# Performance work log

Measured on AMD Instinct MI355X. Metric: run time of the kernel, lower is better.

## Reference

```python
import jax, jax.numpy as jnp
import numpy as np

N_NODES = 100000
N_REL = 8
N_EDGES = 80000
IN_F, HID, OUT = 128, 32, 2
N_GRAPHS = 64


def setup_inputs() -> dict:
    key = jax.random.key(0)
    ks = jax.random.split(key, 12)
    x = jax.random.normal(ks[0], (N_NODES, IN_F), dtype=jnp.float32)
    src = jax.random.randint(ks[1], (N_REL, N_EDGES), 0, N_NODES, dtype=jnp.int32)
    dst = jax.random.randint(ks[2], (N_REL, N_EDGES), 0, N_NODES, dtype=jnp.int32)
    graph_ids = jax.random.randint(ks[3], (N_NODES,), 0, N_GRAPHS, dtype=jnp.int32)
    W1 = jax.random.normal(ks[4], (N_REL, IN_F, HID), dtype=jnp.float32) / np.sqrt(IN_F)
    b1 = jnp.zeros((N_REL, HID), dtype=jnp.float32)
    W2 = jax.random.normal(ks[5], (N_REL, HID, HID), dtype=jnp.float32) / np.sqrt(HID)
    b2 = jnp.zeros((N_REL, HID), dtype=jnp.float32)
    Wc = jax.random.normal(ks[6], (HID, OUT), dtype=jnp.float32) / np.sqrt(HID)
    bc = jnp.zeros((OUT,), dtype=jnp.float32)
    return {"x": x, "src": src, "dst": dst, "graph_ids": graph_ids,
            "num_graphs": N_GRAPHS, "W1": W1, "b1": b1, "W2": W2, "b2": b2,
            "Wc": Wc, "bc": bc}


def _hetero_conv(h, src, dst, W, b, n_nodes):
    """HeteroGraphConv(sum) of per-relation GraphConv(norm='both')."""
    n_rel = W.shape[0]
    out = jnp.zeros((n_nodes, W.shape[2]), dtype=h.dtype)
    ones_e = jnp.ones((src.shape[1],), dtype=h.dtype)
    for r in range(n_rel):  # small fixed relation set
        s, d = src[r], dst[r]
        # symmetric normalization with degree clamped to >= 1 (DGL behavior)
        deg_out = jnp.maximum(jax.ops.segment_sum(ones_e, s, num_segments=n_nodes), 1.0)
        deg_in = jnp.maximum(jax.ops.segment_sum(ones_e, d, num_segments=n_nodes), 1.0)
        hn = h * jax.lax.rsqrt(deg_out)[:, None]      # [N, F_in]
        hw = hn @ W[r]                                # project first (F_in >= F_out)
        agg = jax.ops.segment_sum(hw[s], d, num_segments=n_nodes)  # scatter-sum to dst
        out = out + agg * jax.lax.rsqrt(deg_in)[:, None] + b[r]
    return out


def reference(x, src, dst, graph_ids, num_graphs, W1, b1, W2, b2, Wc, bc):
    n = x.shape[0]
    h = jax.nn.relu(_hetero_conv(x, src, dst, W1, b1, n))
    h = _hetero_conv(h, src, dst, W2, b2, n)
    # per-graph mean pooling over nodes
    sums = jax.ops.segment_sum(h, graph_ids, num_segments=num_graphs)
    cnts = jnp.maximum(jax.ops.segment_sum(jnp.ones((n,), h.dtype), graph_ids,
                                           num_segments=num_graphs), 1.0)
    pooled = sums / cnts[:, None]
    return pooled @ Wc + bc
```

## Files before the change

kernel.cpp:

```cpp
#include <hip/hip_runtime.h>


#define N_NODES 100000
#define N_REL   8
#define N_EDGES 80000
#define IN_F    128
#define HID     32
#define N_GRAPHS 64
#define NCAT    (N_REL * HID)
#define N_KEYS  (N_NODES * N_REL)
#define TOT_E   (N_REL * N_EDGES)
#define DEG_BLOCKS  (TOT_E / 256)
#define GEMM_BLOCKS ((N_NODES / 16 + 3) / 4)
#define GID_BLOCKS  ((N_NODES + 1023) / 1024)

constexpr int TILE = 256;
constexpr int KC   = 32;

typedef __attribute__((ext_vector_type(8))) short bf16x8;
typedef __attribute__((ext_vector_type(4))) float f32x4;

__device__ __forceinline__ ushort f2bf(float v) {
  unsigned u = __builtin_bit_cast(unsigned, v);
  u = (u + 0x7fffu + ((u >> 16) & 1u)) >> 16;
  return (ushort)u;
}
__device__ __forceinline__ float bf2f(ushort h) {
  unsigned u = ((unsigned)h) << 16;
  return __builtin_bit_cast(float, u);
}

__global__ __launch_bounds__(256) void rsqrt_kernel(float* __restrict__ p, int count) {
  int i = blockIdx.x * 256 + threadIdx.x;
  if (i < count) {
    int d = ((const int*)p)[i];
    p[i] = rsqrtf((float)(d < 1 ? 1 : d));
  }
}

__global__ __launch_bounds__(256) void prep_w_kernel(const float* __restrict__ W1, const float* __restrict__ W2,
                                                     const float* __restrict__ Wc,
                                                     ushort* __restrict__ Wt1, ushort* __restrict__ Vt) {
  int i = blockIdx.x * 256 + threadIdx.x;
  if (i < NCAT * IN_F) {
    int n = i >> 7, k = i & 127;
    int r = n >> 5, j = n & 31;
    Wt1[i] = f2bf(W1[r * (IN_F * HID) + k * HID + j]);
  } else {
    int q = i - NCAT * IN_F;
    if (q < 16 * HID) {
      int n = q >> 5, k = q & 31;
      int r = n >> 1, c = n & 1;
      float s = 0.f;
#pragma unroll
      for (int j = 0; j < HID; j++) s += W2[r * (HID * HID) + k * HID + j] * Wc[j * 2 + c];
      Vt[q] = f2bf(s);
    }
  }
}

__global__ __launch_bounds__(256, 4) void fused_deg_gemm1(const int* __restrict__ src, const int* __restrict__ dst,
                                                          int* __restrict__ dego, int* __restrict__ cnt,
                                                          int* __restrict__ epos,
                                                          const float* __restrict__ A, const ushort* __restrict__ Bt,
                                                          ushort* __restrict__ Y, int M,
                                                          const int* __restrict__ gid, float* __restrict__ gcnt) {
  __shared__ ushort smem[17408];
  int bid = blockIdx.x;
  int role, rid;
  if (bid < 2 * GEMM_BLOCKS) { role = bid & 1; rid = bid >> 1; }
  else if (bid < GEMM_BLOCKS + DEG_BLOCKS) { role = 1; rid = GEMM_BLOCKS + (bid - 2 * GEMM_BLOCKS); }
  else { role = 2; rid = bid - (GEMM_BLOCKS + DEG_BLOCKS); }

  if (role == 1) {
    int i = rid * 256 + (int)threadIdx.x;
    int s = src[i], d = dst[i];
    int r = i / N_EDGES;
    atomicAdd(&dego[r * N_NODES + s], 1);
    epos[i] = atomicAdd(&cnt[d * N_REL + r], 1);
    return;
  }
  if (role == 2) {
    int* gh = (int*)smem;
    int t = threadIdx.x;
    if (t < N_GRAPHS) gh[t] = 0;
    __syncthreads();
    int base = rid * 1024;
#pragma unroll
    for (int k = 0; k < 4; k++) {
      int n = base + k * 256 + t;
      if (n < N_NODES) atomicAdd(&gh[gid[n]], 1);
    }
    __syncthreads();
    if (t < N_GRAPHS) atomicAdd(&gcnt[t], (float)gh[t]);
    return;
  }

  int wave = __builtin_amdgcn_readfirstlane(threadIdx.x >> 6);
  int lane = threadIdx.x & 63;
  int t = threadIdx.x;
  int m0 = (rid * 4 + wave) * 16;
  int me = (m0 <= M - 16) ? m0 : (M - 16);
  int row = lane & 15, quad = lane >> 4;

  bf16x8 af[4];
#pragma unroll
  for (int kq = 0; kq < 4; kq++) {
    const float* ap = &A[(size_t)(me + row) * IN_F + kq * 32 + quad * 8];
    float4 a0 = *(const float4*)ap;
    float4 a1 = *(const float4*)(ap + 4);
    bf16x8 a;
    a[0] = (short)f2bf(a0.x); a[1] = (short)f2bf(a0.y); a[2] = (short)f2bf(a0.z); a[3] = (short)f2bf(a0.w);
    a[4] = (short)f2bf(a1.x); a[5] = (short)f2bf(a1.y); a[6] = (short)f2bf(a1.z); a[7] = (short)f2bf(a1.w);
    af[kq] = a;
  }

  f32x4 acc[16];
#pragma unroll
  for (int nt = 0; nt < 16; nt++) acc[nt] = (f32x4){0.f, 0.f, 0.f, 0.f};

  for (int p = 0; p < 2; p++) {
    __syncthreads();
    const ushort* bsrc = Bt + (size_t)p * (128 * IN_F);
#pragma unroll
    for (int i = 0; i < 8; i++) {
      int c = t + i * 256;
      int rr2 = c >> 4, cc = c & 15;
      uint4 v = *(const uint4*)&bsrc[rr2 * IN_F + cc * 8];
      *(uint4*)&smem[rr2 * 136 + cc * 8] = v;
    }
    __syncthreads();
#pragma unroll
    for (int kq = 0; kq < 4; kq++) {
#pragma unroll
      for (int nt2 = 0; nt2 < 8; nt2++) {
        bf16x8 b = *(const bf16x8*)&smem[(nt2 * 16 + row) * 136 + kq * 32 + quad * 8];
        acc[p * 8 + nt2] = __builtin_amdgcn_mfma_f32_16x16x32_bf16(af[kq], b, acc[p * 8 + nt2], 0, 0, 0);
      }
    }
  }
  __syncthreads();

  ushort* myt = &smem[wave * 4160];
#pragma unroll
  for (int nt = 0; nt < 16; nt++) {
#pragma unroll
    for (int i = 0; i < 4; i++)
      myt[(quad * 4 + i) * 260 + nt * 16 + row] = f2bf(acc[nt][i]);
  }
  if (m0 <= M - 16) {
    ushort* ybase = &Y[(size_t)m0 * NCAT];
#pragma unroll
    for (int k = 0; k < 8; k++) {
      int g = k * 512 + lane * 8;
      int r2 = g >> 8, c2 = g & 255;
      const ushort* sp = &myt[r2 * 260 + c2];
      uint4 v;
      v.x = *(const uint*)(sp + 0);
      v.y = *(const uint*)(sp + 2);
      v.z = *(const uint*)(sp + 4);
      v.w = *(const uint*)(sp + 6);
      *(uint4*)&ybase[g] = v;
    }
  }
}

__global__ __launch_bounds__(256) void scan1_kernel(const int* __restrict__ in, int* __restrict__ out,
                                                    int* __restrict__ partial, int n) {
  __shared__ int ts[256];
  int b0 = blockIdx.x * 1024;
  int t = threadIdx.x;
  int v[4]; int s = 0;
#pragma unroll
  for (int k = 0; k < 4; k++) {
    int idx = b0 + t * 4 + k;
    v[k] = s;
    s += (idx < n) ? in[idx] : 0;
  }
  ts[t] = s;
  __syncthreads();
  for (int off = 1; off < 256; off <<= 1) {
    int xv = (t >= off) ? ts[t - off] : 0;
    __syncthreads();
    ts[t] += xv;
    __syncthreads();
  }
  int texcl = (t == 0) ? 0 : ts[t - 1];
#pragma unroll
  for (int k = 0; k < 4; k++) {
    int idx = b0 + t * 4 + k;
    if (idx < n) out[idx] = texcl + v[k];
  }
  if (t == 255) {
    partial[blockIdx.x] = ts[255];
    if (b0 + 1024 >= n) out[n] = ts[255];
  }
}

__global__ __launch_bounds__(256) void scan2_kernel(int* __restrict__ partial, int nb) {
  __shared__ int ts[256];
  int t = threadIdx.x;
  int v[4]; int s = 0;
#pragma unroll
  for (int k = 0; k < 4; k++) {
    int idx = t * 4 + k;
    v[k] = s;
    s += (idx < nb) ? partial[idx] : 0;
  }
  ts[t] = s;
  __syncthreads();
  for (int off = 1; off < 256; off <<= 1) {
    int xv = (t >= off) ? ts[t - off] : 0;
    __syncthreads();
    ts[t] += xv;
    __syncthreads();
  }
  int texcl = (t == 0) ? 0 : ts[t - 1];
#pragma unroll
  for (int k = 0; k < 4; k++) {
    int idx = t * 4 + k;
    if (idx < nb) partial[idx] = texcl + v[k];
  }
}

__global__ __launch_bounds__(256) void fill_kernel(const int* __restrict__ src, const int* __restrict__ dst,
                                                   const int* __restrict__ rp, const int* __restrict__ part,
                                                   const int* __restrict__ epos, const int* __restrict__ dego,
                                                   int4* __restrict__ edata) {
  int i = blockIdx.x * 256 + threadIdx.x;
  int d = dst[i];
  int s = src[i];
  int r = i / N_EDGES;
  int key = d * N_REL + r;
  int b = rp[key] + part[key >> 10];
  int k1 = key + 1;
  int e2 = rp[k1] + part[k1 >> 10];
  int c = e2 - b;
  int t = b + epos[i];
  int dg = dego[r * N_NODES + s];
  float w = rsqrtf((float)(dg < 1 ? 1 : dg)) * rsqrtf((float)(c < 1 ? 1 : c));
  int4 e;
  e.x = s * NCAT + r * HID;
  e.y = __builtin_bit_cast(int, w);
  e.z = d;
  e.w = 0;
  edata[t] = e;
}

__global__ __launch_bounds__(256) void gather1_kernel(const ushort* __restrict__ Ys, const int4* __restrict__ edata,
                                                      const int* __restrict__ rp, const int* __restrict__ part,
                                                      const float* __restrict__ b1, const ushort* __restrict__ Vt,
                                                      float* __restrict__ Ys2) {
  int wave = __builtin_amdgcn_readfirstlane(threadIdx.x >> 6);
  int lane = threadIdx.x & 63;
  int d = blockIdx.x * 4 + wave;
  if (d >= N_NODES) return;
  int j = lane & 31, half = lane >> 5;
  int k0 = d * N_REL, k1 = k0 + N_REL;
  int base = rp[k0] + part[k0 >> 10];
  int endp = rp[k1] + part[k1 >> 10];
  float sum = 0.f;
  for (int t = base + half; t < endp; t += 2) {
    int4 e = edata[t];
    float w = __builtin_bit_cast(float, e.y);
    sum += w * bf2f(Ys[(size_t)e.x + j]);
  }
  sum += __shfl_down(sum, 32);
  float sb = 0.f;
#pragma unroll
  for (int q = 0; q < N_REL; q++) sb += b1[q * HID + j];
  float h = fmaxf(sum + sb, 0.f);
  bf16x8 vrow[4];
  if (lane < 16) {
#pragma unroll
    for (int q = 0; q < 4; q++) vrow[q] = *(const bf16x8*)&Vt[lane * HID + q * 8];
  } else {
#pragma unroll
    for (int q = 0; q < 4; q++) vrow[q] = (bf16x8){0,0,0,0,0,0,0,0};
  }
  float acc = 0.f;
#pragma unroll
  for (int jj = 0; jj < 32; jj++) {
    float hv = __shfl(h, jj);
    acc += hv * bf2f((ushort)vrow[jj >> 3][jj & 7]);
  }
  if (lane < 16) Ys2[(size_t)d * 16 + lane] = acc;
}

__global__ __launch_bounds__(256) void gather2_pool_kernel(const float* __restrict__ Ys2,
                                                           const int4* __restrict__ edata,
                                                           const int* __restrict__ gid,
                                                           float* __restrict__ gpool) {
  __shared__ float lp[N_GRAPHS * 2];
  int t = threadIdx.x;
  if (t < N_GRAPHS * 2) lp[t] = 0.f;
  __syncthreads();
  for (int sidx = blockIdx.x * 256 + t; sidx < TOT_E; sidx += gridDim.x * 256) {
    int4 e = edata[sidx];
    float w = __builtin_bit_cast(float, e.y);
    float2 y = *(const float2*)&Ys2[e.x >> 4];
    int g = gid[e.z];
    atomicAdd(&lp[g * 2 + 0], w * y.x);
    atomicAdd(&lp[g * 2 + 1], w * y.y);
  }
  __syncthreads();
  if (t < N_GRAPHS * 2) atomicAdd(&gpool[t], lp[t]);
}

__global__ void final_kernel(const float* __restrict__ gpool, const float* __restrict__ gcnt,
                             const float* __restrict__ b2, const float* __restrict__ Wc,
                             const float* __restrict__ bc, float* __restrict__ out) {
  int g = threadIdx.x;
  if (g >= N_GRAPHS) return;
  float c0 = 0.f, c1 = 0.f;
#pragma unroll
  for (int k = 0; k < HID; k++) {
    float sb = 0.f;
#pragma unroll
    for (int r = 0; r < N_REL; r++) sb += b2[r * HID + k];
    c0 += sb * Wc[k * 2 + 0];
    c1 += sb * Wc[k * 2 + 1];
  }
  float cntv = gcnt[g];
  if (cntv > 0.f) {
    out[g * 2 + 0] = gpool[g * 2 + 0] / cntv + c0 + bc[0];
    out[g * 2 + 1] = gpool[g * 2 + 1] / cntv + c1 + bc[1];
  } else {
    out[g * 2 + 0] = bc[0];
    out[g * 2 + 1] = bc[1];
  }
}

__global__ __launch_bounds__(256) void deg_kernel(const int* __restrict__ src, const int* __restrict__ dst,
                                                  int* __restrict__ dego, int* __restrict__ degi, int n_rel) {
  int i = blockIdx.x * 256 + threadIdx.x;
  if (i < n_rel * N_EDGES) {
    int r = i / N_EDGES;
    atomicAdd(&dego[r * N_NODES + src[i]], 1);
    atomicAdd(&degi[r * N_NODES + dst[i]], 1);
  }
}

__global__ __launch_bounds__(256) void proj1_kernel(const float* __restrict__ x, const float* __restrict__ W1r0,
                                                    const float* __restrict__ rs_o, float* __restrict__ hw,
                                                    int n0, int n1, int hw_nodes) {
  int rr = blockIdx.y;
  int nb = n0 + blockIdx.x * TILE;
  int t = threadIdx.x;
  __shared__ float xs[TILE][KC + 4];
  const float* __restrict__ Wr = W1r0 + (size_t)rr * (IN_F * HID);
  float acc[HID];
#pragma unroll
  for (int j = 0; j < HID; j++) acc[j] = 0.f;
  for (int kc = 0; kc < IN_F; kc += KC) {
    __syncthreads();
#pragma unroll
    for (int i = 0; i < (TILE * KC / 4) / 256; i++) {
      int q = t + i * 256;
      int nn = q >> 3, k4 = q & 7;
      int n = nb + nn;
      float4 v = make_float4(0.f, 0.f, 0.f, 0.f);
      if (n < n1) v = *(const float4*)&x[(size_t)n * IN_F + kc + k4 * 4];
      *(float4*)&xs[nn][k4 * 4] = v;
    }
    __syncthreads();
#pragma unroll
    for (int k4 = 0; k4 < KC / 4; k4++) {
      float4 xv = *(const float4*)&xs[t][k4 * 4];
      const float* wk = &Wr[(kc + k4 * 4) * HID];
#pragma unroll
      for (int j = 0; j < HID; j++) acc[j] += xv.x * wk[j];
#pragma unroll
      for (int j = 0; j < HID; j++) acc[j] += xv.y * wk[HID + j];
#pragma unroll
      for (int j = 0; j < HID; j++) acc[j] += xv.z * wk[2 * HID + j];
#pragma unroll
      for (int j = 0; j < HID; j++) acc[j] += xv.w * wk[3 * HID + j];
    }
  }
  int n = nb + t;
  if (n < n1) {
    float s = rs_o[(size_t)rr * N_NODES + n];
    float* o = &hw[((size_t)rr * hw_nodes + (n - n0)) * HID];
#pragma unroll
    for (int j4 = 0; j4 < HID / 4; j4++) {
      float4 v = make_float4(acc[j4 * 4] * s, acc[j4 * 4 + 1] * s, acc[j4 * 4 + 2] * s, acc[j4 * 4 + 3] * s);
      *(float4*)&o[j4 * 4] = v;
    }
  }
}

__global__ __launch_bounds__(256) void proj2_kernel(const float* __restrict__ acc1, const float* __restrict__ b1,
                                                    const float* __restrict__ W2r0, const float* __restrict__ rs_o,
                                                    float* __restrict__ hw, int n0, int n1, int hw_nodes) {
  int n = n0 + blockIdx.x * 256 + threadIdx.x;
  if (n >= n1) return;
  int rr = blockIdx.y;
  float h1[HID];
#pragma unroll
  for (int j4 = 0; j4 < HID / 4; j4++) {
    float4 v = *(const float4*)&acc1[(size_t)n * HID + j4 * 4];
    h1[j4 * 4 + 0] = v.x; h1[j4 * 4 + 1] = v.y; h1[j4 * 4 + 2] = v.z; h1[j4 * 4 + 3] = v.w;
  }
#pragma unroll
  for (int j = 0; j < HID; j++) {
    float sb = 0.f;
#pragma unroll
    for (int q = 0; q < N_REL; q++) sb += b1[q * HID + j];
    h1[j] = fmaxf(h1[j] + sb, 0.f);
  }
  const float* __restrict__ Wr = W2r0 + (size_t)rr * (HID * HID);
  float acc[HID];
#pragma unroll
  for (int j = 0; j < HID; j++) acc[j] = 0.f;
#pragma unroll
  for (int k = 0; k < HID; k++) {
    float hv = h1[k];
#pragma unroll
    for (int j = 0; j < HID; j++) acc[j] += hv * Wr[k * HID + j];
  }
  float s = rs_o[(size_t)rr * N_NODES + n];
  float* o = &hw[((size_t)rr * hw_nodes + (n - n0)) * HID];
#pragma unroll
  for (int j4 = 0; j4 < HID / 4; j4++) {
    float4 v = make_float4(acc[j4 * 4] * s, acc[j4 * 4 + 1] * s, acc[j4 * 4 + 2] * s, acc[j4 * 4 + 3] * s);
    *(float4*)&o[j4 * 4] = v;
  }
}

__global__ __launch_bounds__(256) void scatter_kernel(const float* __restrict__ hw, const int* __restrict__ src,
                                                      const int* __restrict__ dst, const float* __restrict__ rs_i,
                                                      float* __restrict__ acc, int nr, int n0, int n1, int hw_nodes) {
  long i = (long)blockIdx.x * 256 + threadIdx.x;
  long total = (long)nr * N_EDGES * HID;
  if (i >= total) return;
  int j = (int)(i & (HID - 1));
  long e = i >> 5;
  int rr = (int)(e / N_EDGES);
  int ee = (int)(e - (long)rr * N_EDGES);
  int s = src[rr * N_EDGES + ee];
  if (s < n0 || s >= n1) return;
  int d = dst[rr * N_EDGES + ee];
  float v = hw[((size_t)rr * hw_nodes + (s - n0)) * HID + j] * rs_i[(size_t)rr * N_NODES + d];
  atomicAdd(&acc[(size_t)d * HID + j], v);
}

__global__ __launch_bounds__(256) void pool_kernel(const float* __restrict__ acc2, const float* __restrict__ b2,
                                                   const int* __restrict__ gid, float* __restrict__ gpool,
                                                   float* __restrict__ gcnt) {
  __shared__ float lp[N_GRAPHS * HID];
  __shared__ float lc[N_GRAPHS];
  int t = threadIdx.x;
  for (int i = t; i < N_GRAPHS * HID; i += 256) lp[i] = 0.f;
  if (t < N_GRAPHS) lc[t] = 0.f;
  __syncthreads();
  int j = t & (HID - 1);
  int grp = t >> 5;
  float sb = 0.f;
#pragma unroll
  for (int q = 0; q < N_REL; q++) sb += b2[q * HID + j];
  for (int n = blockIdx.x * 8 + grp; n < N_NODES; n += gridDim.x * 8) {
    int g = gid[n];
    float v = acc2[(size_t)n * HID + j] + sb;
    atomicAdd(&lp[g * HID + j], v);
    if (j == 0) atomicAdd(&lc[g], 1.f);
  }
  __syncthreads();
  for (int i = t; i < N_GRAPHS * HID; i += 256) atomicAdd(&gpool[i], lp[i]);
  if (t < N_GRAPHS) atomicAdd(&gcnt[t], lc[t]);
}

__global__ void final3_kernel(const float* __restrict__ gpool, const float* __restrict__ gcnt,
                              const float* __restrict__ Wc, const float* __restrict__ bc,
                              float* __restrict__ out) {
  int g = threadIdx.x;
  if (g >= N_GRAPHS) return;
  float inv = 1.f / fmaxf(gcnt[g], 1.f);
  float o0 = bc[0], o1 = bc[1];
#pragma unroll
  for (int k = 0; k < HID; k++) {
    float p = gpool[g * HID + k] * inv;
    o0 += p * Wc[k * 2 + 0];
    o1 += p * Wc[k * 2 + 1];
  }
  out[g * 2 + 0] = o0;
  out[g * 2 + 1] = o1;
}

extern "C" void kernel_launch(void* const* d_in, const int* in_sizes, int n_in,
                              void* d_out, int out_size, void* d_ws, size_t ws_size,
                              hipStream_t stream) {
  const float* x  = (const float*)d_in[0];
  const int* src  = (const int*)d_in[1];
  const int* dst  = (const int*)d_in[2];
  const int* gid  = (const int*)d_in[3];
  const float* W1 = (const float*)d_in[5];
  const float* b1 = (const float*)d_in[6];
  const float* W2 = (const float*)d_in[7];
  const float* b2 = (const float*)d_in[8];
  const float* Wc = (const float*)d_in[9];
  const float* bc = (const float*)d_in[10];
  float* out = (float*)d_out;

  float* ws = (float*)d_ws;
  const size_t NF = (size_t)N_NODES * HID;
  const size_t RN = (size_t)N_REL * N_NODES;
  const size_t POOLF = N_GRAPHS * HID + N_GRAPHS;
  size_t wsf = ws_size / 4;

  const size_t T1_NEED = 22500000;

  if (wsf >= T1_NEED) {
    float* gpool = ws;
    float* gcnt  = gpool + N_GRAPHS * 2;
    int*   dego  = (int*)(gcnt + N_GRAPHS);
    int*   cnt   = dego + RN;
    int*   epos  = cnt + N_KEYS;
    int*   rp    = epos + TOT_E;
    int*   part  = rp + N_KEYS + 8;
    int4*  edata = (int4*)(part + 1024);
    float* Ys2   = (float*)(edata + TOT_E);
    ushort* Ys   = (ushort*)(Ys2 + (size_t)N_NODES * 16);
    ushort* Wt1  = Ys + (size_t)N_NODES * NCAT;
    ushort* Vt   = Wt1 + NCAT * IN_F;

    size_t zbytes = (N_GRAPHS * 3 + RN + (size_t)N_KEYS) * 4;
    hipMemsetAsync(ws, 0, zbytes, stream);

    prep_w_kernel<<<(NCAT * IN_F + 16 * HID + 255) / 256, 256, 0, stream>>>(W1, W2, Wc, Wt1, Vt);
    fused_deg_gemm1<<<DEG_BLOCKS + GEMM_BLOCKS + GID_BLOCKS, 256, 0, stream>>>(src, dst, dego, cnt, epos,
                                                                               x, Wt1, Ys, N_NODES, gid, gcnt);

    int sblocks = (N_KEYS + 1023) / 1024;
    scan1_kernel<<<sblocks, 256, 0, stream>>>(cnt, rp, part, N_KEYS);
    scan2_kernel<<<1, 256, 0, stream>>>(part, sblocks);
    fill_kernel<<<TOT_E / 256, 256, 0, stream>>>(src, dst, rp, part, epos, dego, edata);

    int nblocks = (N_NODES + 3) / 4;
    gather1_kernel<<<nblocks, 256, 0, stream>>>(Ys, edata, rp, part, b1, Vt, Ys2);
    gather2_pool_kernel<<<416, 256, 0, stream>>>(Ys2, edata, gid, gpool);
    final_kernel<<<1, 64, 0, stream>>>(gpool, gcnt, b2, Wc, bc, out);
  } else {
    float* acc1  = ws;
    float* acc2  = acc1 + NF;
    float* gpool = acc2 + NF;
    float* gcnt  = gpool + N_GRAPHS * HID;
    float* rsb   = ws + (2 * NF + POOLF);
    size_t zf = 2 * NF + POOLF;
    float* rs_o = rsb;
    float* rs_i = rsb + N_NODES;
    float* hw = rsb + 2 * N_NODES;
    size_t fixed3 = zf + 2 * N_NODES;
    size_t avail = (wsf > fixed3) ? (wsf - fixed3) : 0;
    long chunk = (long)(avail / HID) & ~255L;
    if (chunk < 256) chunk = 256;
    if (chunk > N_NODES) chunk = N_NODES;

    size_t zb = zf * 4; if (zb > ws_size) zb = ws_size;
    hipMemsetAsync(d_ws, 0, zb, stream);

    for (int layer = 0; layer < 2; layer++) {
      for (int r = 0; r < N_REL; r++) {
        hipMemsetAsync(rs_o, 0, 2 * N_NODES * 4, stream);
        deg_kernel<<<(N_EDGES + 255) / 256, 256, 0, stream>>>(src + (size_t)r * N_EDGES, dst + (size_t)r * N_EDGES,
                                                              (int*)rs_o, (int*)rs_i, 1);
        rsqrt_kernel<<<(2 * N_NODES + 255) / 256, 256, 0, stream>>>(rs_o, 2 * N_NODES);
        for (long n0 = 0; n0 < N_NODES; n0 += chunk) {
          long n1 = n0 + chunk; if (n1 > N_NODES) n1 = N_NODES;
          int tiles = (int)((n1 - n0 + TILE - 1) / TILE);
          if (layer == 0)
            proj1_kernel<<<dim3(tiles, 1), 256, 0, stream>>>(x, W1 + (size_t)r * IN_F * HID, rs_o, hw,
                                                             (int)n0, (int)n1, (int)chunk);
          else
            proj2_kernel<<<dim3(tiles, 1), 256, 0, stream>>>(acc1, b1, W2 + (size_t)r * HID * HID, rs_o, hw,
                                                             (int)n0, (int)n1, (int)chunk);
          long tot = (long)N_EDGES * HID;
          scatter_kernel<<<(int)((tot + 255) / 256), 256, 0, stream>>>(hw, src + (size_t)r * N_EDGES,
                                                                       dst + (size_t)r * N_EDGES, rs_i,
                                                                       layer == 0 ? acc1 : acc2,
                                                                       1, (int)n0, (int)n1, (int)chunk);
        }
      }
    }
    pool_kernel<<<256, 256, 0, stream>>>(acc2, b2, gid, gpool, gcnt);
    final3_kernel<<<1, 64, 0, stream>>>(gpool, gcnt, Wc, bc, out);
  }
}
```

Before: 258.7 us.

## Process 64 destination nodes per block in gather1 with shared-memory atomic accumulation

The first-layer gather now assigns a contiguous range of 64 destination nodes to each block instead of one node per wave. Threads stride over that whole CSR edge range, read two bf16 features per lane, and accumulate into a shared-memory tile with LDS atomics. Bias, ReLU and the 32x16 second projection then run from shared memory with weights held in registers. This is meant to fix the load imbalance and idle lanes of one-wave-per-node (about 6.4 edges per node on average), at the cost of LDS atomic contention and extra block barriers.

```diff
diff --git a/kernel.cpp b/kernel.cpp
--- a/kernel.cpp
+++ b/kernel.cpp
@@ -13,6 +13,7 @@
 #define DEG_BLOCKS  (TOT_E / 256)
 #define GEMM_BLOCKS ((N_NODES / 16 + 3) / 4)
 #define GID_BLOCKS  ((N_NODES + 1023) / 1024)
+#define G1_NB 64
 
 constexpr int TILE = 256;
 constexpr int KC   = 32;
@@ -251,40 +252,62 @@
                                                       const int* __restrict__ rp, const int* __restrict__ part,
                                                       const float* __restrict__ b1, const ushort* __restrict__ Vt,
                                                       float* __restrict__ Ys2) {
-  int wave = __builtin_amdgcn_readfirstlane(threadIdx.x >> 6);
-  int lane = threadIdx.x & 63;
-  int d = blockIdx.x * 4 + wave;
-  if (d >= N_NODES) return;
-  int j = lane & 31, half = lane >> 5;
-  int k0 = d * N_REL, k1 = k0 + N_REL;
+  __shared__ float h[G1_NB][33];
+  __shared__ float sbias[HID];
+  int t = threadIdx.x;
+  int d0 = blockIdx.x * G1_NB;
+  int d1 = d0 + G1_NB; if (d1 > N_NODES) d1 = N_NODES;
+  for (int i = t; i < G1_NB * 33; i += 256) (&h[0][0])[i] = 0.f;
+  if (t < HID) {
+    float sb = 0.f;
+#pragma unroll
+    for (int q = 0; q < N_REL; q++) sb += b1[q * HID + t];
+    sbias[t] = sb;
+  }
+  __syncthreads();
+
+  int k0 = d0 * N_REL, k1e = d1 * N_REL;
   int base = rp[k0] + part[k0 >> 10];
-  int endp = rp[k1] + part[k1 >> 10];
-  float sum = 0.f;
-  for (int t = base + half; t < endp; t += 2) {
-    int4 e = edata[t];
+  int endp = rp[k1e] + part[k1e >> 10];
+
+  int g = t >> 4;
+  int j2 = (t & 15) * 2;
+  for (int s = base + g; s < endp; s += 16) {
+    int4 e = edata[s];
     float w = __builtin_bit_cast(float, e.y);
-    sum += w * bf2f(Ys[(size_t)e.x + j]);
-  }
-  sum += __shfl_down(sum, 32);
-  float sb = 0.f;
-#pragma unroll
-  for (int q = 0; q < N_REL; q++) sb += b1[q * HID + j];
-  float h = fmaxf(sum + sb, 0.f);
-  bf16x8 vrow[4];
-  if (lane < 16) {
-#pragma unroll
-    for (int q = 0; q < 4; q++) vrow[q] = *(const bf16x8*)&Vt[lane * HID + q * 8];
-  } else {
-#pragma unroll
-    for (int q = 0; q < 4; q++) vrow[q] = (bf16x8){0,0,0,0,0,0,0,0};
-  }
-  float acc = 0.f;
-#pragma unroll
-  for (int jj = 0; jj < 32; jj++) {
-    float hv = __shfl(h, jj);
-    acc += hv * bf2f((ushort)vrow[jj >> 3][jj & 7]);
-  }
-  if (lane < 16) Ys2[(size_t)d * 16 + lane] = acc;
+    uint yy = *(const uint*)&Ys[(size_t)e.x + j2];
+    float y0 = bf2f((ushort)(yy & 0xffffu));
+    float y1 = bf2f((ushort)(yy >> 16));
+    int dl = e.z - d0;
+    atomicAdd(&h[dl][j2], w * y0);
+    atomicAdd(&h[dl][j2 + 1], w * y1);
+  }
+  __syncthreads();
+
+  for (int i = t; i < G1_NB * HID; i += 256) {
+    int ln = i >> 5, k = i & 31;
+    h[ln][k] = fmaxf(h[ln][k] + sbias[k], 0.f);
+  }
+  __syncthreads();
+
+  int ln = t >> 4, c = t & 15;
+  float vreg[HID];
+#pragma unroll
+  for (int q = 0; q < 4; q++) {
+    bf16x8 v = *(const bf16x8*)&Vt[c * HID + q * 8];
+#pragma unroll
+    for (int m = 0; m < 8; m++) vreg[q * 8 + m] = bf2f((ushort)v[m]);
+  }
+#pragma unroll
+  for (int nb = 0; nb < G1_NB; nb += 16) {
+    int d = d0 + nb + ln;
+    if (d < d1) {
+      float acc = 0.f;
+#pragma unroll
+      for (int k = 0; k < HID; k++) acc += h[nb + ln][k] * vreg[k];
+      Ys2[(size_t)d * 16 + c] = acc;
+    }
+  }
 }
 
 __global__ __launch_bounds__(256) void gather2_pool_kernel(const float* __restrict__ Ys2,
@@ -536,8 +559,8 @@
     scan2_kernel<<<1, 256, 0, stream>>>(part, sblocks);
     fill_kernel<<<TOT_E / 256, 256, 0, stream>>>(src, dst, rp, part, epos, dego, edata);
 
-    int nblocks = (N_NODES + 3) / 4;
-    gather1_kernel<<<nblocks, 256, 0, stream>>>(Ys, edata, rp, part, b1, Vt, Ys2);
+    int g1blocks = (N_NODES + G1_NB - 1) / G1_NB;
+    gather1_kernel<<<g1blocks, 256, 0, stream>>>(Ys, edata, rp, part, b1, Vt, Ys2);
     gather2_pool_kernel<<<416, 256, 0, stream>>>(Ys2, edata, gid, gpool);
     final_kernel<<<1, 64, 0, stream>>>(gpool, gcnt, b2, Wc, bc, out);
   } else {
```

Result: slower. 329.9 us (+27.5%).
